# Kernel tuning notes

Hardware: AMD Instinct MI355X
Metric: run time of the kernel (lower is better)

Reference implementation:

```python
import jax, jax.numpy as jnp
import numpy as np

OUT, IN, GS = 16384, 4096, 16
G = OUT * IN // GS  # 4194304 groups


def setup_inputs() -> dict:
    key = jax.random.key(0)
    k1, k2, k3, k4 = jax.random.split(key, 4)
    x = jax.random.normal(k1, (8, 32, IN), dtype=jnp.float32)
    weight_q2 = jax.random.randint(k2, (G, GS // 4), 0, 256, dtype=jnp.int32)
    weight_norm = jax.random.uniform(k3, (G, 1), dtype=jnp.float16)
    bias = jax.random.normal(k4, (OUT,), dtype=jnp.float32)
    return {"x": x, "weight_q2": weight_q2, "weight_norm": weight_norm, "bias": bias}


def _dequant_2bit(weight_q2, weight_norm):
    # torch: xq_out[:, i::4] = (xq >> 2i) & 3  =>  element index within group = i + 4*k
    # where k = packed column (slow, stride 4), i = shift index (fast).
    norm = weight_norm.astype(jnp.float32)                      # [G, 1]
    shifts = jnp.arange(4, dtype=jnp.int32) * 2                 # [4]
    vals = (weight_q2[:, :, None] >> shifts) & 3                # [G, 4(pack k), 4(shift i)]
    xq_out = vals.astype(jnp.float32).reshape(G, GS)            # [G, 16], layout k*4 + i
    w = (xq_out / 3.0) * (2.0 * norm) - norm                    # [G, 16]
    return w.reshape(OUT, IN)


def reference(x, weight_q2, weight_norm, bias):
    w = _dequant_2bit(weight_q2, weight_norm)                   # [OUT, IN] fp32
    return jnp.einsum('bsi,oi->bso', x, w) + bias
```

## Files before the change

### kernel.cpp

```cpp
#include <hip/hip_runtime.h>
#include <stdint.h>

#define M_DIM 256
#define N_DIM 16384
#define K_DIM 4096
#define BM 128
#define BN 64
#define BK 64

typedef __bf16 bf16x8 __attribute__((ext_vector_type(8)));
typedef float  f32x4  __attribute__((ext_vector_type(4)));

__device__ __forceinline__ uint32_t f2bf(float f) {
  uint32_t u = __float_as_uint(f);
  return (u + 0x7fffu + ((u >> 16) & 1u)) >> 16;
}

__global__ __launch_bounds__(256) void cvt_x_kernel(const float* __restrict__ x,
                                                    uint4* __restrict__ ws) {
  int T = blockIdx.x * 256 + threadIdx.x;
  int mb_glob = T >> 13;
  int r       = T & 8191;
  int kch     = r >> 6;
  int L       = r & 63;
  int row = mb_glob * 16 + (L & 15);
  int k   = kch * 32 + (L >> 4) * 8;
  const float* p = x + (size_t)row * K_DIM + k;
  float4 a = *(const float4*)p;
  float4 b = *(const float4*)(p + 4);
  uint4 o;
  o.x = f2bf(a.x) | (f2bf(a.y) << 16);
  o.y = f2bf(a.z) | (f2bf(a.w) << 16);
  o.z = f2bf(b.x) | (f2bf(b.y) << 16);
  o.w = f2bf(b.z) | (f2bf(b.w) << 16);
  ws[T] = o;
}

__global__ __launch_bounds__(256, 2) void gemm2bit_kernel(
    const uint4*    __restrict__ aws,
    const uint32_t* __restrict__ q2,
    const float*    __restrict__ nrm,
    const float*    __restrict__ bias,
    float*          __restrict__ out)
{
  __shared__ uint4 Ab[1024];
  __shared__ uint4 Bb[512];

  const int tid  = threadIdx.x;
  const int lane = tid & 63;
  const int w    = tid >> 6;
  const int wm   = w >> 1;
  const int wn   = w & 1;
  const int lo4  = lane & 15;
  const int qd   = lane >> 4;

  const int n0 = blockIdx.x * BN;
  const int m0 = blockIdx.y * BM;

  const int snb  = tid >> 6;
  const int sqd  = (tid >> 4) & 3;
  const int slo4 = tid & 15;
  const int grow = n0 + snb * 16 + slo4;

  f32x4 acc[4][2];
#pragma unroll
  for (int s = 0; s < 4; ++s)
#pragma unroll
    for (int u = 0; u < 2; ++u)
      acc[s][u] = (f32x4){0.f, 0.f, 0.f, 0.f};

  for (int kc = 0; kc < K_DIM; kc += BK) {
    __syncthreads();

#pragma unroll
    for (int j = 0; j < 4; ++j) {
      int s_lin = j * 256 + tid;
      int ca = s_lin >> 6;
      int L  = s_lin & 63;
      int ts = ca >> 3, mb = ca & 7;
      uint4 g = aws[((size_t)(blockIdx.y * 8 + mb) * 128 + (kc >> 5) + ts) * 64 + L];
      Ab[ca * 64 + L] = g;
    }

    {
      int gidx = grow * 256 + (kc >> 4) + sqd;
      uint4 q  = *(const uint4*)(q2 + (size_t)gidx * 4);
      float nv = nrm[gidx];
      float a  = nv * (2.0f / 3.0f);
      float b  = -nv;
      uint32_t res[8];
#pragma unroll
      for (int p = 0; p < 4; ++p) {
        uint32_t qq = (&q.x)[p];
        float f0 = fmaf((float)(qq & 3u), a, b);
        float f1 = fmaf((float)((qq >> 2) & 3u), a, b);
        float f2 = fmaf((float)((qq >> 4) & 3u), a, b);
        float f3 = fmaf((float)((qq >> 6) & 3u), a, b);
        res[p * 2]     = f2bf(f0) | (f2bf(f1) << 16);
        res[p * 2 + 1] = f2bf(f2) | (f2bf(f3) << 16);
      }
      int cb   = (sqd >> 1) * 4 + snb;
      int base = cb * 64 + (sqd & 1) * 32 + slo4;
      Bb[base]      = make_uint4(res[0], res[1], res[2], res[3]);
      Bb[base + 16] = make_uint4(res[4], res[5], res[6], res[7]);
    }

    __syncthreads();

#pragma unroll
    for (int ts = 0; ts < 2; ++ts) {
      bf16x8 af[4], bf[2];
#pragma unroll
      for (int s = 0; s < 4; ++s)
        af[s] = *(const bf16x8*)&Ab[(ts * 8 + wm * 4 + s) * 64 + lane];
#pragma unroll
      for (int u = 0; u < 2; ++u)
        bf[u] = *(const bf16x8*)&Bb[(ts * 4 + wn * 2 + u) * 64 + lane];
#pragma unroll
      for (int s = 0; s < 4; ++s)
#pragma unroll
        for (int u = 0; u < 2; ++u)
          acc[s][u] = __builtin_amdgcn_mfma_f32_16x16x32_bf16(
              af[s], bf[u], acc[s][u], 0, 0, 0);
    }
  }

  float bv[2];
#pragma unroll
  for (int u = 0; u < 2; ++u)
    bv[u] = bias[n0 + wn * 32 + u * 16 + lo4];

#pragma unroll
  for (int s = 0; s < 4; ++s) {
    int mrow = m0 + wm * 64 + s * 16 + qd * 4;
#pragma unroll
    for (int u = 0; u < 2; ++u) {
      int ncol = n0 + wn * 32 + u * 16 + lo4;
      float* p = out + (size_t)mrow * N_DIM + ncol;
#pragma unroll
      for (int r = 0; r < 4; ++r)
        p[(size_t)r * N_DIM] = acc[s][u][r] + bv[u];
    }
  }
}

extern "C" void kernel_launch(void* const* d_in, const int* in_sizes, int n_in,
                              void* d_out, int out_size, void* d_ws, size_t ws_size,
                              hipStream_t stream) {
  const float*    x    = (const float*)d_in[0];
  const uint32_t* q2   = (const uint32_t*)d_in[1];
  const float*    nm   = (const float*)d_in[2];
  const float*    bias = (const float*)d_in[3];
  float*          out  = (float*)d_out;
  uint4*          aws  = (uint4*)d_ws;

  cvt_x_kernel<<<512, 256, 0, stream>>>(x, aws);

  dim3 grid(N_DIM / BN, M_DIM / BM);
  gemm2bit_kernel<<<grid, 256, 0, stream>>>(aws, q2, nm, bias, out);
}
```

Baseline: 178.6 us.

## Restructure 2-bit GEMM into per-warp pipelined tiles with LUT-based perm dequant

```diff
diff --git a/kernel.cpp b/kernel.cpp
--- a/kernel.cpp
+++ b/kernel.cpp
@@ -4,9 +4,7 @@
 #define M_DIM 256
 #define N_DIM 16384
 #define K_DIM 4096
-#define BM 128
-#define BN 64
-#define BK 64
+#define NT 64
 
 typedef __bf16 bf16x8 __attribute__((ext_vector_type(8)));
 typedef float  f32x4  __attribute__((ext_vector_type(4)));
@@ -36,6 +34,20 @@
   ws[T] = o;
 }
 
+__device__ __forceinline__ uint4 deq8(uint32_t qx, uint32_t qy, uint32_t tlo,
+                                      uint32_t thi) {
+  uint32_t s0 = ((qx & 3u) | ((qx & 0xCu) << 14)) * 0x0202u + 0x01000100u;
+  uint32_t s1 = (((qx >> 4) & 3u) | ((qx & 0xC0u) << 10)) * 0x0202u + 0x01000100u;
+  uint32_t s2 = ((qy & 3u) | ((qy & 0xCu) << 14)) * 0x0202u + 0x01000100u;
+  uint32_t s3 = (((qy >> 4) & 3u) | ((qy & 0xC0u) << 10)) * 0x0202u + 0x01000100u;
+  uint4 r;
+  r.x = __builtin_amdgcn_perm(thi, tlo, s0);
+  r.y = __builtin_amdgcn_perm(thi, tlo, s1);
+  r.z = __builtin_amdgcn_perm(thi, tlo, s2);
+  r.w = __builtin_amdgcn_perm(thi, tlo, s3);
+  return r;
+}
+
 __global__ __launch_bounds__(256, 2) void gemm2bit_kernel(
     const uint4*    __restrict__ aws,
     const uint32_t* __restrict__ q2,
@@ -43,103 +55,128 @@
     const float*    __restrict__ bias,
     float*          __restrict__ out)
 {
-  __shared__ uint4 Ab[1024];
-  __shared__ uint4 Bb[512];
+  __shared__ uint4 Sc[4][2][256];
 
   const int tid  = threadIdx.x;
   const int lane = tid & 63;
   const int w    = tid >> 6;
-  const int wm   = w >> 1;
-  const int wn   = w & 1;
   const int lo4  = lane & 15;
   const int qd   = lane >> 4;
+  const int rr   = lane & 31;
+  const int khi  = lane >> 5;
+  const int n0w  = blockIdx.x * 128 + w * 32;
+  const int m0   = blockIdx.y * 64;
 
-  const int n0 = blockIdx.x * BN;
-  const int m0 = blockIdx.y * BM;
+  uint4 (*scr)[256] = Sc[w];
 
-  const int snb  = tid >> 6;
-  const int sqd  = (tid >> 4) & 3;
-  const int slo4 = tid & 15;
-  const int grow = n0 + snb * 16 + slo4;
+  const uint4* pA = aws + (size_t)(blockIdx.y * 4) * 8192 + lane;
+
+  const uint32_t* pq = q2 + ((size_t)(n0w + rr) * 256 + khi * 2) * 4;
+  const float*    pn = nrm + (size_t)(n0w + rr) * 256;
+
+  const int wbase = (lane >> 4) * 64 + lo4;
 
   f32x4 acc[4][2];
 #pragma unroll
-  for (int s = 0; s < 4; ++s)
+  for (int mc = 0; mc < 4; ++mc)
 #pragma unroll
     for (int u = 0; u < 2; ++u)
-      acc[s][u] = (f32x4){0.f, 0.f, 0.f, 0.f};
+      acc[mc][u] = (f32x4){0.f, 0.f, 0.f, 0.f};
 
-  for (int kc = 0; kc < K_DIM; kc += BK) {
-    __syncthreads();
+#define DEQ_WRITE(PP, Q1, Q2v, N4)                                             \
+  do {                                                                         \
+    float nv1 = khi ? (N4).z : (N4).x;                                         \
+    float nv2 = khi ? (N4).w : (N4).y;                                         \
+    float a1 = nv1 * (2.0f / 3.0f);                                            \
+    uint32_t t1lo = f2bf(-nv1) | (f2bf(fmaf(1.0f, a1, -nv1)) << 16);           \
+    uint32_t t1hi = f2bf(fmaf(2.0f, a1, -nv1)) |                               \
+                    (f2bf(fmaf(3.0f, a1, -nv1)) << 16);                        \
+    scr[PP][wbase]      = deq8((Q1).x, (Q1).y, t1lo, t1hi);                    \
+    scr[PP][wbase + 16] = deq8((Q1).z, (Q1).w, t1lo, t1hi);                    \
+    float a2 = nv2 * (2.0f / 3.0f);                                            \
+    uint32_t t2lo = f2bf(-nv2) | (f2bf(fmaf(1.0f, a2, -nv2)) << 16);           \
+    uint32_t t2hi = f2bf(fmaf(2.0f, a2, -nv2)) |                               \
+                    (f2bf(fmaf(3.0f, a2, -nv2)) << 16);                        \
+    scr[PP][wbase + 32] = deq8((Q2v).x, (Q2v).y, t2lo, t2hi);                  \
+    scr[PP][wbase + 48] = deq8((Q2v).z, (Q2v).w, t2lo, t2hi);                  \
+  } while (0)
+
+  uint4 afE[8], afO[8];
+  uint4 qA1, qA2, qB1, qB2;
+  float4 nA4, nB4;
 
 #pragma unroll
-    for (int j = 0; j < 4; ++j) {
-      int s_lin = j * 256 + tid;
-      int ca = s_lin >> 6;
-      int L  = s_lin & 63;
-      int ts = ca >> 3, mb = ca & 7;
-      uint4 g = aws[((size_t)(blockIdx.y * 8 + mb) * 128 + (kc >> 5) + ts) * 64 + L];
-      Ab[ca * 64 + L] = g;
-    }
+  for (int mc = 0; mc < 4; ++mc)
+#pragma unroll
+    for (int ts = 0; ts < 2; ++ts)
+      afE[mc * 2 + ts] = pA[(size_t)mc * 8192 + ts * 64];
+  {
+    uint4 q01 = *(const uint4*)pq;
+    uint4 q02 = *(const uint4*)(pq + 4);
+    float4 n04 = *(const float4*)pn;
+    qA1 = *(const uint4*)(pq + 16);  qA2 = *(const uint4*)(pq + 20);
+    nA4 = *(const float4*)(pn + 4);
+    qB1 = *(const uint4*)(pq + 32);  qB2 = *(const uint4*)(pq + 36);
+    nB4 = *(const float4*)(pn + 8);
+    DEQ_WRITE(0, q01, q02, n04);
+  }
+  asm volatile("s_waitcnt lgkmcnt(0)" ::: "memory");
+  __builtin_amdgcn_sched_barrier(0);
 
-    {
-      int gidx = grow * 256 + (kc >> 4) + sqd;
-      uint4 q  = *(const uint4*)(q2 + (size_t)gidx * 4);
-      float nv = nrm[gidx];
-      float a  = nv * (2.0f / 3.0f);
-      float b  = -nv;
-      uint32_t res[8];
-#pragma unroll
-      for (int p = 0; p < 4; ++p) {
-        uint32_t qq = (&q.x)[p];
-        float f0 = fmaf((float)(qq & 3u), a, b);
-        float f1 = fmaf((float)((qq >> 2) & 3u), a, b);
-        float f2 = fmaf((float)((qq >> 4) & 3u), a, b);
-        float f3 = fmaf((float)((qq >> 6) & 3u), a, b);
-        res[p * 2]     = f2bf(f0) | (f2bf(f1) << 16);
-        res[p * 2 + 1] = f2bf(f2) | (f2bf(f3) << 16);
-      }
-      int cb   = (sqd >> 1) * 4 + snb;
-      int base = cb * 64 + (sqd & 1) * 32 + slo4;
-      Bb[base]      = make_uint4(res[0], res[1], res[2], res[3]);
-      Bb[base + 16] = make_uint4(res[4], res[5], res[6], res[7]);
-    }
+#define BODY(T, PP, AFC, AFN, Q1, Q2v, N4)                                     \
+  do {                                                                         \
+    if ((T) + 1 < NT) {                                                        \
+      _Pragma("unroll")                                                        \
+      for (int mc = 0; mc < 4; ++mc)                                           \
+        _Pragma("unroll")                                                      \
+        for (int ts = 0; ts < 2; ++ts)                                         \
+          AFN[mc * 2 + ts] = pA[(size_t)mc * 8192 + (((T) + 1) * 2 + ts) * 64];\
+    }                                                                          \
+    bf16x8 bfv[4];                                                             \
+    _Pragma("unroll")                                                          \
+    for (int c = 0; c < 4; ++c)                                                \
+      bfv[c] = *(const bf16x8*)&scr[PP][c * 64 + lane];                        \
+    if ((T) + 1 < NT) DEQ_WRITE((PP) ^ 1, Q1, Q2v, N4);                        \
+    if ((T) + 3 < NT) {                                                        \
+      Q1  = *(const uint4*)(pq + ((T) + 3) * 16);                              \
+      Q2v = *(const uint4*)(pq + ((T) + 3) * 16 + 4);                          \
+      N4  = *(const float4*)(pn + ((T) + 3) * 4);                              \
+    }                                                                          \
+    _Pragma("unroll")                                                          \
+    for (int mc = 0; mc < 4; ++mc)                                             \
+      _Pragma("unroll")                                                        \
+      for (int ts = 0; ts < 2; ++ts) {                                         \
+        bf16x8 av = __builtin_bit_cast(bf16x8, AFC[mc * 2 + ts]);              \
+        _Pragma("unroll")                                                      \
+        for (int u = 0; u < 2; ++u)                                            \
+          acc[mc][u] = __builtin_amdgcn_mfma_f32_16x16x32_bf16(av,             \
+                           bfv[ts * 2 + u], acc[mc][u], 0, 0, 0);              \
+      }                                                                        \
+    asm volatile("s_waitcnt lgkmcnt(0)" ::: "memory");                         \
+    __builtin_amdgcn_sched_barrier(0);                                         \
+  } while (0)
 
-    __syncthreads();
-
-#pragma unroll
-    for (int ts = 0; ts < 2; ++ts) {
-      bf16x8 af[4], bf[2];
-#pragma unroll
-      for (int s = 0; s < 4; ++s)
-        af[s] = *(const bf16x8*)&Ab[(ts * 8 + wm * 4 + s) * 64 + lane];
-#pragma unroll
-      for (int u = 0; u < 2; ++u)
-        bf[u] = *(const bf16x8*)&Bb[(ts * 4 + wn * 2 + u) * 64 + lane];
-#pragma unroll
-      for (int s = 0; s < 4; ++s)
-#pragma unroll
-        for (int u = 0; u < 2; ++u)
-          acc[s][u] = __builtin_amdgcn_mfma_f32_16x16x32_bf16(
-              af[s], bf[u], acc[s][u], 0, 0, 0);
-    }
+  for (int t2 = 0; t2 < NT; t2 += 2) {
+    BODY(t2,     0, afE, afO, qA1, qA2, nA4);
+    BODY(t2 + 1, 1, afO, afE, qB1, qB2, nB4);
   }
+#undef BODY
+#undef DEQ_WRITE
 
   float bv[2];
 #pragma unroll
   for (int u = 0; u < 2; ++u)
-    bv[u] = bias[n0 + wn * 32 + u * 16 + lo4];
-
+    bv[u] = bias[n0w + u * 16 + lo4];
 #pragma unroll
-  for (int s = 0; s < 4; ++s) {
-    int mrow = m0 + wm * 64 + s * 16 + qd * 4;
+  for (int mc = 0; mc < 4; ++mc) {
+    int mrow = m0 + mc * 16 + qd * 4;
 #pragma unroll
     for (int u = 0; u < 2; ++u) {
-      int ncol = n0 + wn * 32 + u * 16 + lo4;
+      int ncol = n0w + u * 16 + lo4;
       float* p = out + (size_t)mrow * N_DIM + ncol;
 #pragma unroll
       for (int r = 0; r < 4; ++r)
-        p[(size_t)r * N_DIM] = acc[s][u][r] + bv[u];
+        p[(size_t)r * N_DIM] = acc[mc][u][r] + bv[u];
     }
   }
 }
@@ -155,7 +192,6 @@
   uint4*          aws  = (uint4*)d_ws;
 
   cvt_x_kernel<<<512, 256, 0, stream>>>(x, aws);
-
-  dim3 grid(N_DIM / BN, M_DIM / BM);
-  gemm2bit_kernel<<<grid, 256, 0, stream>>>(aws, q2, nm, bias, out);
+  gemm2bit_kernel<<<dim3(N_DIM / 128, M_DIM / 64), 256, 0, stream>>>(
+      aws, q2, nm, bias, out);
 }
```

Measured after the change: 195.0 us. 1.09x slower.
